# Performance work log

Measured on AMD Instinct MI355X. Metric: run time of the kernel, lower is better.

The kernel has to match this reference:

```python
import jax, jax.numpy as jnp
import numpy as np

T = 8           # hardcoded frame count in forward
MAX_D = 3       # hardcoded displacement radius -> 7x7 = 49-entry cost volume
PATCH = 2 * MAX_D + 1
EPS = 1e-12     # F.normalize eps


def _l2norm_c(x):
    # x: [B, C, H, W]; L2-normalize over channel dim (torch F.normalize dim=1)
    n = jnp.sqrt(jnp.sum(x * x, axis=1, keepdims=True))
    return x / jnp.maximum(n, EPS)


def setup_inputs() -> dict:
    key = jax.random.key(0)
    ks = jax.random.split(key, 6)
    B, N, C = 2, 8192, 512
    nh = 8
    d = C // nh
    return {
        "x": jax.random.normal(ks[0], (B, N, C), jnp.float32),
        "w_qk": jax.random.normal(ks[1], (2 * C, C), jnp.float32) * 0.02,
        "w_corr": jax.random.normal(ks[2], (d, PATCH * PATCH), jnp.float32) * 0.02,
        "b_corr": jax.random.normal(ks[3], (d,), jnp.float32) * 0.02,
        "w_proj": jax.random.normal(ks[4], (C, C), jnp.float32) * 0.02,
        "b_proj": jax.random.normal(ks[5], (C,), jnp.float32) * 0.02,
    }


def reference(x, w_qk, w_corr, b_corr, w_proj, b_proj):
    B, N, C = x.shape
    nh = 8
    d = C // nh
    H = int(round((N // T) ** 0.5))
    W = H

    # qk projection (no bias): [B, N, 2C] -> [2, B, nh, N, d]
    qk = jnp.einsum('bnc,ec->bne', x, w_qk).reshape(B, N, 2, nh, d)
    q = jnp.transpose(qk[:, :, 0], (0, 2, 1, 3))  # [B, nh, N, d]
    k = jnp.transpose(qk[:, :, 1], (0, 2, 1, 3))

    # 'b n (t h w) d -> (b n) t d h w'
    def to_vid(a):
        a = a.reshape(B, nh, T, H, W, d)
        return jnp.transpose(a, (0, 1, 2, 5, 3, 4)).reshape(B * nh, T, d, H, W)

    q = to_vid(q)
    k = to_vid(k)

    # k_postfix: shift time forward, repeat last frame
    k_post = jnp.concatenate([k[:, 1:], k[:, -1:]], axis=1)

    BT = B * nh * T
    qf = _l2norm_c(q.reshape(BT, d, H, W))
    kf = _l2norm_c(k_post.reshape(BT, d, H, W))

    # local cost volume: corr[b, u*7+v, y, x] = sum_c qf[b,c,y,x] * kf[b,c,y+u-3,x+v-3]
    kp = jnp.pad(kf, ((0, 0), (0, 0), (MAX_D, MAX_D), (MAX_D, MAX_D)))
    corr = jnp.stack(
        [jnp.sum(qf * kp[:, :, u:u + H, v:v + W], axis=1)
         for u in range(PATCH) for v in range(PATCH)],
        axis=1,
    )  # [BT, 49, H, W]

    # 'b u v h w -> b (h w) (u v)'
    corr = jnp.transpose(corr, (0, 2, 3, 1)).reshape(BT, H * W, PATCH * PATCH)

    # proj_corr: 49 -> head_dim
    mf = jnp.einsum('bpk,dk->bpd', corr, w_corr) + b_corr  # [BT, HW, d]

    # '(b n t) (h w) d -> b (t h w) (n d)'
    mf = mf.reshape(B, nh, T, H, W, d)
    mf = jnp.transpose(mf, (0, 2, 3, 4, 1, 5)).reshape(B, N, C)

    # final projection
    return jnp.einsum('bnc,oc->bno', mf, w_proj) + b_proj
```

## Files before the change

kernel.cpp:

```cpp
#include <hip/hip_runtime.h>

typedef unsigned int u32;
typedef unsigned short u16;
typedef __fp16 h2 __attribute__((ext_vector_type(2)));
typedef __fp16 f16x8 __attribute__((ext_vector_type(8)));
typedef float f32x4 __attribute__((ext_vector_type(4)));

#define DEVFN static __device__ __forceinline__

DEVFN u32 pkh(float a, float b) {
  return __builtin_bit_cast(u32, __builtin_amdgcn_cvt_pkrtz(a, b));
}
DEVFN u16 f2h(float f) { __fp16 h = (__fp16)f; return __builtin_bit_cast(u16, h); }

#if __has_builtin(__builtin_amdgcn_fdot2)
DEVFN float dot2u(u32 a, u32 b, float c) {
  return __builtin_amdgcn_fdot2(__builtin_bit_cast(h2, a),
                                __builtin_bit_cast(h2, b), c, false);
}
#else
DEVFN float dot2u(u32 a, u32 b, float c) {
  h2 x = __builtin_bit_cast(h2, a), y = __builtin_bit_cast(h2, b);
  return c + (float)x[0] * (float)y[0] + (float)x[1] * (float)y[1];
}
#endif

DEVFN uint4 pk8(f32x4 lo, f32x4 hi) {
  uint4 o;
  o.x = pkh(lo.x, lo.y); o.y = pkh(lo.z, lo.w);
  o.z = pkh(hi.x, hi.y); o.w = pkh(hi.z, hi.w);
  return o;
}

DEVFN void gld16(const u16* g, u16* l) {
  __builtin_amdgcn_global_load_lds(
      (const __attribute__((address_space(1))) u32*)g,
      (__attribute__((address_space(3))) u32*)l, 16, 0, 0);
}

DEVFN void waitl0() { asm volatile("s_waitcnt lgkmcnt(0)" ::: "memory"); }
DEVFN void rbar() {
  __builtin_amdgcn_sched_barrier(0);
  __builtin_amdgcn_s_barrier();
  __builtin_amdgcn_sched_barrier(0);
}

__global__ __launch_bounds__(512) void gemm1(
    const float* __restrict__ Af, const float* __restrict__ Bf,
    u16* __restrict__ Out, int Nn, int K) {
  __shared__ u16 As[2][4096];
  __shared__ u16 Bs[2][16384];
  const int tid = threadIdx.x;
  const int lane = tid & 63;
  const int w = tid >> 6;
  const int wm = w >> 2, wn = w & 3;
  const int nwg = (int)gridDim.x;
  const int wg = ((int)blockIdx.x & 7) * (nwg >> 3) + ((int)blockIdx.x >> 3);
  const int tm = wg >> 1, tn = wg & 1;

  const int ra = tid >> 2;
  const int s8 = (tid & 3) << 3;
  const size_t offA = (size_t)(tm * 128 + ra) * K + s8;
  const size_t offB = (size_t)(tn * 512 + ra) * K + s8;
  const int wofs = ra * 32 + s8;

  const int rofsA = ((wm * 64 + (lane & 15)) << 5) + ((lane >> 4) << 3);
  const int rofsB = ((wn * 128 + (lane & 15)) << 5) + ((lane >> 4) << 3);

  f32x4 acc[4][8] = {};
  f32x4 a0, a1, b0, b1, b2, b3, b4, b5, b6, b7;

#define LOADF(t)                                                          \
  {                                                                       \
    const size_t oa = offA + (size_t)(t) * 32;                            \
    const size_t ob = offB + (size_t)(t) * 32;                            \
    a0 = *(const f32x4*)(Af + oa);                                        \
    a1 = *(const f32x4*)(Af + oa + 4);                                    \
    b0 = *(const f32x4*)(Bf + ob);                                        \
    b1 = *(const f32x4*)(Bf + ob + 4);                                    \
    b2 = *(const f32x4*)(Bf + ob + (size_t)128 * K);                      \
    b3 = *(const f32x4*)(Bf + ob + (size_t)128 * K + 4);                  \
    b4 = *(const f32x4*)(Bf + ob + (size_t)256 * K);                      \
    b5 = *(const f32x4*)(Bf + ob + (size_t)256 * K + 4);                  \
    b6 = *(const f32x4*)(Bf + ob + (size_t)384 * K);                      \
    b7 = *(const f32x4*)(Bf + ob + (size_t)384 * K + 4);                  \
  }
#define WRITEF(bufi)                                                      \
  {                                                                       \
    *(uint4*)(&As[bufi][wofs]) = pk8(a0, a1);                             \
    *(uint4*)(&Bs[bufi][wofs]) = pk8(b0, b1);                             \
    *(uint4*)(&Bs[bufi][wofs + 4096]) = pk8(b2, b3);                      \
    *(uint4*)(&Bs[bufi][wofs + 8192]) = pk8(b4, b5);                      \
    *(uint4*)(&Bs[bufi][wofs + 12288]) = pk8(b6, b7);                     \
  }

  const int KT = K >> 5;
  LOADF(0)
  WRITEF(0)
  LOADF(1)
  waitl0();
  rbar();
  for (int kt = 0; kt < KT; ++kt) {
    const int cur = kt & 1;
    f16x8 af[4], bf[8];
#pragma unroll
    for (int i = 0; i < 4; ++i) af[i] = *(const f16x8*)(&As[cur][rofsA + i * 512]);
#pragma unroll
    for (int i = 0; i < 8; ++i) bf[i] = *(const f16x8*)(&Bs[cur][rofsB + i * 512]);
    if (kt + 1 < KT) {
      WRITEF(cur ^ 1)
      if (kt + 2 < KT) LOADF(kt + 2)
    }
    __builtin_amdgcn_s_setprio(1);
#pragma unroll
    for (int mi = 0; mi < 4; ++mi)
#pragma unroll
      for (int ni = 0; ni < 8; ++ni)
        acc[mi][ni] = __builtin_amdgcn_mfma_f32_16x16x32_f16(af[mi], bf[ni],
                                                             acc[mi][ni], 0, 0, 0);
    __builtin_amdgcn_s_setprio(0);
    waitl0();
    rbar();
  }
#undef LOADF
#undef WRITEF

  const int rowBase = tm * 128 + wm * 64 + ((lane >> 4) << 2);
  const int colLo = tn * 512 + wn * 128;
  const int colHi = colLo + 64;
  const int selLo = colLo >> 9, hhLo = (colLo >> 6) & 7;
  const int selHi = colHi >> 9, hhHi = (colHi >> 6) & 7;
  const int ddb = lane & 15;
#pragma unroll
  for (int mi = 0; mi < 4; ++mi)
#pragma unroll
    for (int r = 0; r < 4; ++r) {
      float sl = acc[mi][0][r] * acc[mi][0][r] + acc[mi][1][r] * acc[mi][1][r] +
                 acc[mi][2][r] * acc[mi][2][r] + acc[mi][3][r] * acc[mi][3][r];
      float sh = acc[mi][4][r] * acc[mi][4][r] + acc[mi][5][r] * acc[mi][5][r] +
                 acc[mi][6][r] * acc[mi][6][r] + acc[mi][7][r] * acc[mi][7][r];
      sl += __shfl_xor(sl, 1); sh += __shfl_xor(sh, 1);
      sl += __shfl_xor(sl, 2); sh += __shfl_xor(sh, 2);
      sl += __shfl_xor(sl, 4); sh += __shfl_xor(sh, 4);
      sl += __shfl_xor(sl, 8); sh += __shfl_xor(sh, 8);
      float invl = 1.0f / fmaxf(sqrtf(sl), 1e-12f);
      float invh = 1.0f / fmaxf(sqrtf(sh), 1e-12f);
      const int m = rowBase + mi * 16 + r;
      const int bb = m >> 13, tt = (m >> 10) & 7, pix = m & 1023;
      const size_t pxo = (size_t)pix * 64 + ddb;
      const int frL = ((selLo * 2 + bb) * 8 + tt) * 8 + hhLo;
      const int frH = ((selHi * 2 + bb) * 8 + tt) * 8 + hhHi;
      size_t baseL = (((size_t)frL) << 16) + pxo;
      size_t baseH = (((size_t)frH) << 16) + pxo;
#pragma unroll
      for (int ni = 0; ni < 4; ++ni) {
        Out[baseL + ni * 16] = f2h(acc[mi][ni][r] * invl);
        Out[baseH + ni * 16] = f2h(acc[mi][ni + 4][r] * invh);
      }
    }
}

__global__ __launch_bounds__(256) void gemm2b(
    const u16* __restrict__ A, const u16* __restrict__ B,
    const float* __restrict__ bias, float* __restrict__ Out,
    int Nn, int K) {
  __shared__ u16 As[2][2048];
  __shared__ u16 Bs[2][4096];
  const int tid = threadIdx.x;
  const int lane = tid & 63;
  const int w = tid >> 6;
  const int nwg = (int)gridDim.x;
  const int wg = ((int)blockIdx.x & 7) * (nwg >> 3) + ((int)blockIdx.x >> 3);
  const int tm = wg >> 2, tn = wg & 3;

  const u16* gA = A + (size_t)(tm * 64 + w * 16 + (lane >> 2)) * K +
                  ((lane & 3) << 3);
  const u16* gB = B + (size_t)(tn * 128 + w * 32 + (lane >> 2)) * K +
                  ((lane & 3) << 3);

  const int rofsA = ((lane & 15) << 5) + ((lane >> 4) << 3);
  const int rofsB = w * 1024 + ((lane & 15) << 5) + ((lane >> 4) << 3);

  f32x4 acc[4][2] = {};

#define STG(bufi, t)                                                      \
  {                                                                       \
    gld16(gA + (size_t)(t) * 32, &As[bufi][w * 512]);                     \
    gld16(gB + (size_t)(t) * 32, &Bs[bufi][w * 1024]);                    \
    gld16(gB + (size_t)(t) * 32 + (size_t)16 * K, &Bs[bufi][w * 1024 + 512]); \
  }

  const int KT = K >> 6;
  for (int kt = 0; kt < KT; ++kt) {
    __syncthreads();
    STG(0, 2 * kt)
    STG(1, 2 * kt + 1)
    __syncthreads();
#pragma unroll
    for (int sub = 0; sub < 2; ++sub) {
      f16x8 af[4], bf[2];
#pragma unroll
      for (int i = 0; i < 4; ++i)
        af[i] = *(const f16x8*)(&As[sub][rofsA + i * 512]);
#pragma unroll
      for (int i = 0; i < 2; ++i)
        bf[i] = *(const f16x8*)(&Bs[sub][rofsB + i * 512]);
#pragma unroll
      for (int mi = 0; mi < 4; ++mi)
#pragma unroll
        for (int ni = 0; ni < 2; ++ni)
          acc[mi][ni] = __builtin_amdgcn_mfma_f32_16x16x32_f16(
              af[mi], bf[ni], acc[mi][ni], 0, 0, 0);
    }
  }
#undef STG

  const int rowBase = tm * 64 + ((lane >> 4) << 2);
  const int colBase = tn * 128 + w * 32 + (lane & 15);
  float bv[2];
#pragma unroll
  for (int ni = 0; ni < 2; ++ni) bv[ni] = bias[colBase + ni * 16];
#pragma unroll
  for (int mi = 0; mi < 4; ++mi)
#pragma unroll
    for (int r = 0; r < 4; ++r) {
      size_t ro = (size_t)(rowBase + mi * 16 + r) * Nn;
#pragma unroll
      for (int ni = 0; ni < 2; ++ni)
        Out[ro + colBase + ni * 16] = acc[mi][ni][r] + bv[ni];
    }
}

__global__ __launch_bounds__(256) void dots_w2(
    const u16* __restrict__ qf, u16* __restrict__ corr,
    const float* __restrict__ wp, const float* __restrict__ wc,
    const float* __restrict__ bc, const float* __restrict__ bp,
    u16* __restrict__ W2, float* __restrict__ cvec) {
  __shared__ __align__(16) u16 smem[448 * 64];
  const int tid = threadIdx.x;

  if ((int)blockIdx.x >= 512) {
    const int o = (int)blockIdx.x - 512;
    float* wcl = (float*)smem;
    float* wpl = wcl + 3136;
    for (int i = tid; i < 3136; i += 256) wcl[i] = wc[i];
    wpl[tid] = wp[o * 512 + tid];
    wpl[tid + 256] = wp[o * 512 + tid + 256];
    __syncthreads();
#pragma unroll
    for (int pass = 0; pass < 2; ++pass) {
      const int idx = pass * 256 + tid;
      if (idx < 448) {
        const int hh = idx / 56, r = idx % 56, du = r >> 3, dv = r & 7;
        float sv = 0.f;
        if (dv < 7) {
#pragma unroll
          for (int c = 0; c < 64; ++c)
            sv += wpl[hh * 64 + c] * wcl[c * 49 + du * 7 + dv];
        }
        W2[o * 448 + idx] = f2h(sv);
      }
    }
    if (tid < 64) {
      float p = 0.f;
#pragma unroll
      for (int g = 0; g < 8; ++g) p += wpl[g * 64 + tid];
      p *= bc[tid];
      p += __shfl_xor(p, 1); p += __shfl_xor(p, 2); p += __shfl_xor(p, 4);
      p += __shfl_xor(p, 8); p += __shfl_xor(p, 16); p += __shfl_xor(p, 32);
      if (tid == 0) cvec[o] = p + bp[o];
    }
    return;
  }

  u16* kst = smem;
  const int bid = ((int)blockIdx.x & 7) * 64 + ((int)blockIdx.x >> 3);
  const int fr = bid >> 2, grp = bid & 3;
  const int h = fr & 7, t = (fr >> 3) & 7, b = fr >> 6;
  const int t1 = (t < 7) ? t + 1 : 7;
  const int y0 = grp * 8;

  const u16* kbase = qf + (((size_t)(((2 + b) * 8 + t1) * 8 + h)) << 16);
  {
    const int ppx = tid >> 3;
    const int slot = tid & 7;
#pragma unroll
    for (int pass = 0; pass < 14; ++pass) {
      int gy = y0 - 3 + pass;
      uint4 v = make_uint4(0, 0, 0, 0);
      if ((unsigned)gy < 32u)
        v = *(const uint4*)(kbase + (size_t)(gy * 32 + ppx) * 64 + slot * 8);
      int pl = pass * 32 + ppx;
      *(uint4*)((char*)kst + pl * 128 + ((slot * 16) ^ ((pl & 7) << 4))) = v;
    }
  }

  const int px = grp * 256 + tid;
  const int x = tid & 31, yloc = tid >> 5;
  const u16* qp = qf + (((size_t)fr) << 16) + (size_t)px * 64;
  u32 qw[32];
#pragma unroll
  for (int j = 0; j < 8; ++j) {
    uint4 v = *(const uint4*)(qp + j * 8);
    qw[j * 4 + 0] = v.x; qw[j * 4 + 1] = v.y;
    qw[j * 4 + 2] = v.z; qw[j * 4 + 3] = v.w;
  }
  __syncthreads();

  u16* mp = corr + (size_t)((b * 8 + t) * 1024 + px) * 448 + h * 56;
  for (int du = 0; du < 7; ++du) {
    const int rlbase = (yloc + du) * 32;
    float f[7];
#pragma unroll
    for (int dv = 0; dv < 7; ++dv) {
      int xx = x + dv - 3;
      int xc = xx < 0 ? 0 : (xx > 31 ? 31 : xx);
      int pl = rlbase + xc;
      const char* kr = (const char*)kst + pl * 128;
      const int swz = (pl & 7) << 4;
      float s0 = 0.f, s1 = 0.f, s2 = 0.f, s3 = 0.f;
#pragma unroll
      for (int j = 0; j < 8; ++j) {
        uint4 v = *(const uint4*)(kr + ((j * 16) ^ swz));
        s0 = dot2u(qw[j * 4 + 0], v.x, s0);
        s1 = dot2u(qw[j * 4 + 1], v.y, s1);
        s2 = dot2u(qw[j * 4 + 2], v.z, s2);
        s3 = dot2u(qw[j * 4 + 3], v.w, s3);
      }
      float s = (s0 + s1) + (s2 + s3);
      f[dv] = ((unsigned)xx < 32u) ? s : 0.f;
    }
    uint4 o;
    o.x = pkh(f[0], f[1]); o.y = pkh(f[2], f[3]);
    o.z = pkh(f[4], f[5]); o.w = pkh(f[6], 0.f);
    *(uint4*)(mp + du * 8) = o;
  }
}

extern "C" void kernel_launch(void* const* d_in, const int* in_sizes, int n_in,
                              void* d_out, int out_size, void* d_ws, size_t ws_size,
                              hipStream_t stream) {
  const float* x      = (const float*)d_in[0];
  const float* w_qk   = (const float*)d_in[1];
  const float* w_corr = (const float*)d_in[2];
  const float* b_corr = (const float*)d_in[3];
  const float* w_proj = (const float*)d_in[4];
  const float* b_proj = (const float*)d_in[5];
  float* out = (float*)d_out;

  u16* corr = (u16*)d_ws;
  u16* qf   = corr + (size_t)16384 * 448;
  u16* W2   = qf + (size_t)16384 * 1024;
  float* cvec = (float*)(W2 + (size_t)512 * 448);

  gemm1<<<dim3(256), dim3(512), 0, stream>>>(x, w_qk, qf, 1024, 512);
  dots_w2<<<dim3(1024), dim3(256), 0, stream>>>(qf, corr, w_proj, w_corr,
                                                b_corr, b_proj, W2, cvec);
  gemm2b<<<dim3(1024), dim3(256), 0, stream>>>(corr, W2, cvec, out, 512, 448);
}
```

Before: 74.60 us.

## Pre-convert w_qk to fp16 and stage B tiles via global_load_lds

Adds a prep kernel that converts w_qk to fp16 and also does the W2/cvec weight folding, which was previously done inside the dots kernel. gemm1 now reads the fp16 weight and copies B tiles straight into LDS with global_load_lds, so it no longer loads fp32 B through registers, packs it and writes it to LDS. The wait becomes vmcnt(2) so the A prefetch can stay in flight. The cost is an extra launch and extra global traffic each call for the weight conversion. The B tile layout in LDS also changes, which relies on the fragment read offsets still matching it.

Result: slower. 76.74 us (+2.9%).

```diff
diff --git a/kernel.cpp b/kernel.cpp
--- a/kernel.cpp
+++ b/kernel.cpp
@@ -38,16 +38,61 @@
       (__attribute__((address_space(3))) u32*)l, 16, 0, 0);
 }
 
-DEVFN void waitl0() { asm volatile("s_waitcnt lgkmcnt(0)" ::: "memory"); }
 DEVFN void rbar() {
   __builtin_amdgcn_sched_barrier(0);
   __builtin_amdgcn_s_barrier();
   __builtin_amdgcn_sched_barrier(0);
 }
 
+__global__ __launch_bounds__(256) void prep(
+    const float* __restrict__ wp, const float* __restrict__ wc,
+    const float* __restrict__ bc, const float* __restrict__ bp,
+    const float* __restrict__ wqk,
+    u16* __restrict__ W2, float* __restrict__ cvec, u16* __restrict__ wqh) {
+  const int tid = threadIdx.x;
+  if ((int)blockIdx.x >= 512) {
+    const size_t e = ((size_t)((int)blockIdx.x - 512) * 256 + tid) * 8;
+    f32x4 v0 = *(const f32x4*)(wqk + e);
+    f32x4 v1 = *(const f32x4*)(wqk + e + 4);
+    *(uint4*)(wqh + e) = pk8(v0, v1);
+    return;
+  }
+  __shared__ float wcl[64 * 49 + 512];
+  float* wpl = wcl + 3136;
+  const int o = blockIdx.x;
+  for (int i = tid; i < 3136; i += 256) wcl[i] = wc[i];
+  wpl[tid] = wp[o * 512 + tid];
+  wpl[tid + 256] = wp[o * 512 + tid + 256];
+  __syncthreads();
+#pragma unroll
+  for (int pass = 0; pass < 2; ++pass) {
+    const int idx = pass * 256 + tid;
+    if (idx < 448) {
+      const int hh = idx / 56, r = idx % 56, du = r >> 3, dv = r & 7;
+      float sv = 0.f;
+      if (dv < 7) {
+#pragma unroll
+        for (int c = 0; c < 64; ++c)
+          sv += wpl[hh * 64 + c] * wcl[c * 49 + du * 7 + dv];
+      }
+      W2[o * 448 + idx] = f2h(sv);
+    }
+  }
+  if (tid < 64) {
+    float p = 0.f;
+#pragma unroll
+    for (int g = 0; g < 8; ++g) p += wpl[g * 64 + tid];
+    p *= bc[tid];
+    p += __shfl_xor(p, 1); p += __shfl_xor(p, 2); p += __shfl_xor(p, 4);
+    p += __shfl_xor(p, 8); p += __shfl_xor(p, 16); p += __shfl_xor(p, 32);
+    if (tid == 0) cvec[o] = p + bp[o];
+  }
+}
+
 __global__ __launch_bounds__(512) void gemm1(
-    const float* __restrict__ Af, const float* __restrict__ Bf,
-    u16* __restrict__ Out, int Nn, int K) {
+    const float* __restrict__ Af, const u16* __restrict__ Bh,
+    u16* __restrict__ Out) {
+  const int K = 512;
   __shared__ u16 As[2][4096];
   __shared__ u16 Bs[2][16384];
   const int tid = threadIdx.x;
@@ -61,69 +106,79 @@
   const int ra = tid >> 2;
   const int s8 = (tid & 3) << 3;
   const size_t offA = (size_t)(tm * 128 + ra) * K + s8;
-  const size_t offB = (size_t)(tn * 512 + ra) * K + s8;
   const int wofs = ra * 32 + s8;
+
+  const u16* gB = Bh + (size_t)(tn * 512 + w * 64 + (lane >> 2)) * K +
+                  ((lane & 3) << 3);
 
   const int rofsA = ((wm * 64 + (lane & 15)) << 5) + ((lane >> 4) << 3);
   const int rofsB = ((wn * 128 + (lane & 15)) << 5) + ((lane >> 4) << 3);
 
   f32x4 acc[4][8] = {};
-  f32x4 a0, a1, b0, b1, b2, b3, b4, b5, b6, b7;
-
-#define LOADF(t)                                                          \
+  f32x4 a0, a1;
+
+#define LOADA(t)                                                          \
   {                                                                       \
     const size_t oa = offA + (size_t)(t) * 32;                            \
-    const size_t ob = offB + (size_t)(t) * 32;                            \
     a0 = *(const f32x4*)(Af + oa);                                        \
     a1 = *(const f32x4*)(Af + oa + 4);                                    \
-    b0 = *(const f32x4*)(Bf + ob);                                        \
-    b1 = *(const f32x4*)(Bf + ob + 4);                                    \
-    b2 = *(const f32x4*)(Bf + ob + (size_t)128 * K);                      \
-    b3 = *(const f32x4*)(Bf + ob + (size_t)128 * K + 4);                  \
-    b4 = *(const f32x4*)(Bf + ob + (size_t)256 * K);                      \
-    b5 = *(const f32x4*)(Bf + ob + (size_t)256 * K + 4);                  \
-    b6 = *(const f32x4*)(Bf + ob + (size_t)384 * K);                      \
-    b7 = *(const f32x4*)(Bf + ob + (size_t)384 * K + 4);                  \
-  }
-#define WRITEF(bufi)                                                      \
+  }
+#define WRITEA(bufi) { *(uint4*)(&As[bufi][wofs]) = pk8(a0, a1); }
+#define STAGEB(bufi, t)                                                   \
   {                                                                       \
-    *(uint4*)(&As[bufi][wofs]) = pk8(a0, a1);                             \
-    *(uint4*)(&Bs[bufi][wofs]) = pk8(b0, b1);                             \
-    *(uint4*)(&Bs[bufi][wofs + 4096]) = pk8(b2, b3);                      \
-    *(uint4*)(&Bs[bufi][wofs + 8192]) = pk8(b4, b5);                      \
-    *(uint4*)(&Bs[bufi][wofs + 12288]) = pk8(b6, b7);                     \
-  }
+    const u16* gb = gB + (size_t)(t) * 32;                                \
+    gld16(gb, &Bs[bufi][w * 2048]);                                       \
+    gld16(gb + (size_t)16 * K, &Bs[bufi][w * 2048 + 512]);                \
+    gld16(gb + (size_t)32 * K, &Bs[bufi][w * 2048 + 1024]);               \
+    gld16(gb + (size_t)48 * K, &Bs[bufi][w * 2048 + 1536]);               \
+  }
+#define FRAGS(bufi)                                                       \
+  f16x8 af[4], bf[8];                                                     \
+  _Pragma("unroll") for (int i = 0; i < 4; ++i)                           \
+      af[i] = *(const f16x8*)(&As[bufi][rofsA + i * 512]);                \
+  _Pragma("unroll") for (int i = 0; i < 8; ++i)                           \
+      bf[i] = *(const f16x8*)(&Bs[bufi][rofsB + i * 512]);
+#define MFMAS                                                             \
+  __builtin_amdgcn_s_setprio(1);                                          \
+  _Pragma("unroll") for (int mi = 0; mi < 4; ++mi)                        \
+      _Pragma("unroll") for (int ni = 0; ni < 8; ++ni)                    \
+          acc[mi][ni] = __builtin_amdgcn_mfma_f32_16x16x32_f16(           \
+              af[mi], bf[ni], acc[mi][ni], 0, 0, 0);                      \
+  __builtin_amdgcn_s_setprio(0);
+#define WAIT_V2L0 asm volatile("s_waitcnt vmcnt(2) lgkmcnt(0)" ::: "memory");
 
   const int KT = K >> 5;
-  LOADF(0)
-  WRITEF(0)
-  LOADF(1)
-  waitl0();
+  LOADA(0)
+  WRITEA(0)
+  STAGEB(0, 0)
+  __builtin_amdgcn_sched_barrier(0);
+  LOADA(1)
+  __builtin_amdgcn_sched_barrier(0);
+  WAIT_V2L0
   rbar();
+
   for (int kt = 0; kt < KT; ++kt) {
     const int cur = kt & 1;
-    f16x8 af[4], bf[8];
-#pragma unroll
-    for (int i = 0; i < 4; ++i) af[i] = *(const f16x8*)(&As[cur][rofsA + i * 512]);
-#pragma unroll
-    for (int i = 0; i < 8; ++i) bf[i] = *(const f16x8*)(&Bs[cur][rofsB + i * 512]);
+    FRAGS(cur)
     if (kt + 1 < KT) {
-      WRITEF(cur ^ 1)
-      if (kt + 2 < KT) LOADF(kt + 2)
-    }
-    __builtin_amdgcn_s_setprio(1);
-#pragma unroll
-    for (int mi = 0; mi < 4; ++mi)
-#pragma unroll
-      for (int ni = 0; ni < 8; ++ni)
-        acc[mi][ni] = __builtin_amdgcn_mfma_f32_16x16x32_f16(af[mi], bf[ni],
-                                                             acc[mi][ni], 0, 0, 0);
-    __builtin_amdgcn_s_setprio(0);
-    waitl0();
-    rbar();
-  }
-#undef LOADF
-#undef WRITEF
+      WRITEA(cur ^ 1)
+      STAGEB(cur ^ 1, kt + 1)
+      __builtin_amdgcn_sched_barrier(0);
+      LOADA(kt + 2 < KT ? kt + 2 : KT - 1)
+      __builtin_amdgcn_sched_barrier(0);
+    }
+    MFMAS
+    if (kt + 1 < KT) {
+      WAIT_V2L0
+      rbar();
+    }
+  }
+#undef LOADA
+#undef WRITEA
+#undef STAGEB
+#undef FRAGS
+#undef MFMAS
+#undef WAIT_V2L0
 
   const int rowBase = tm * 128 + wm * 64 + ((lane >> 4) << 2);
   const int colLo = tn * 512 + wn * 128;
@@ -231,49 +286,10 @@
     }
 }
 
-__global__ __launch_bounds__(256) void dots_w2(
-    const u16* __restrict__ qf, u16* __restrict__ corr,
-    const float* __restrict__ wp, const float* __restrict__ wc,
-    const float* __restrict__ bc, const float* __restrict__ bp,
-    u16* __restrict__ W2, float* __restrict__ cvec) {
-  __shared__ __align__(16) u16 smem[448 * 64];
+__global__ __launch_bounds__(256) void dots(
+    const u16* __restrict__ qf, u16* __restrict__ corr) {
+  __shared__ __align__(16) u16 kst[448 * 64];
   const int tid = threadIdx.x;
-
-  if ((int)blockIdx.x >= 512) {
-    const int o = (int)blockIdx.x - 512;
-    float* wcl = (float*)smem;
-    float* wpl = wcl + 3136;
-    for (int i = tid; i < 3136; i += 256) wcl[i] = wc[i];
-    wpl[tid] = wp[o * 512 + tid];
-    wpl[tid + 256] = wp[o * 512 + tid + 256];
-    __syncthreads();
-#pragma unroll
-    for (int pass = 0; pass < 2; ++pass) {
-      const int idx = pass * 256 + tid;
-      if (idx < 448) {
-        const int hh = idx / 56, r = idx % 56, du = r >> 3, dv = r & 7;
-        float sv = 0.f;
-        if (dv < 7) {
-#pragma unroll
-          for (int c = 0; c < 64; ++c)
-            sv += wpl[hh * 64 + c] * wcl[c * 49 + du * 7 + dv];
-        }
-        W2[o * 448 + idx] = f2h(sv);
-      }
-    }
-    if (tid < 64) {
-      float p = 0.f;
-#pragma unroll
-      for (int g = 0; g < 8; ++g) p += wpl[g * 64 + tid];
-      p *= bc[tid];
-      p += __shfl_xor(p, 1); p += __shfl_xor(p, 2); p += __shfl_xor(p, 4);
-      p += __shfl_xor(p, 8); p += __shfl_xor(p, 16); p += __shfl_xor(p, 32);
-      if (tid == 0) cvec[o] = p + bp[o];
-    }
-    return;
-  }
-
-  u16* kst = smem;
   const int bid = ((int)blockIdx.x & 7) * 64 + ((int)blockIdx.x >> 3);
   const int fr = bid >> 2, grp = bid & 3;
   const int h = fr & 7, t = (fr >> 3) & 7, b = fr >> 6;
@@ -352,9 +368,11 @@
   u16* qf   = corr + (size_t)16384 * 448;
   u16* W2   = qf + (size_t)16384 * 1024;
   float* cvec = (float*)(W2 + (size_t)512 * 448);
-
-  gemm1<<<dim3(256), dim3(512), 0, stream>>>(x, w_qk, qf, 1024, 512);
-  dots_w2<<<dim3(1024), dim3(256), 0, stream>>>(qf, corr, w_proj, w_corr,
-                                                b_corr, b_proj, W2, cvec);
+  u16* wqh  = (u16*)(cvec + 512);
+
+  prep<<<dim3(768), dim3(256), 0, stream>>>(w_proj, w_corr, b_corr, b_proj,
+                                            w_qk, W2, cvec, wqh);
+  gemm1<<<dim3(256), dim3(512), 0, stream>>>(x, wqh, qf);
+  dots<<<dim3(512), dim3(256), 0, stream>>>(qf, corr);
   gemm2b<<<dim3(1024), dim3(256), 0, stream>>>(corr, W2, cvec, out, 512, 448);
 }
```
